# Performance work log

Measured on AMD Instinct MI355X. Metric: run time of the kernel, lower is better.

## Reference

```python
import jax, jax.numpy as jnp
import numpy as np

# Model dims (see init_kwargs)
E = 512        # embedding_dim
H = 1536       # hidden_dim
SIZE = 4       # state_space.size (state types per layer)
S = 32         # choices per state type (uniform state size)
L = 12         # num_layers of child network
T = SIZE * L   # total controller steps = 48
V = SIZE * S   # num_embeddings = 128


def setup_inputs() -> dict:
    key = jax.random.key(0)
    ks = jax.random.split(key, 12)
    sc = 0.05
    f32 = jnp.float32
    return {
        "input_id": 0,
        "emb":   (jax.random.normal(ks[0], (V, E)) * sc).astype(f32),
        "W_ih1": (jax.random.normal(ks[1], (4 * H, E)) * sc).astype(f32),
        "W_hh1": (jax.random.normal(ks[2], (4 * H, H)) * sc).astype(f32),
        "b_ih1": (jax.random.normal(ks[3], (4 * H,)) * sc).astype(f32),
        "b_hh1": (jax.random.normal(ks[4], (4 * H,)) * sc).astype(f32),
        "W_ih2": (jax.random.normal(ks[5], (4 * H, H)) * sc).astype(f32),
        "W_hh2": (jax.random.normal(ks[6], (4 * H, H)) * sc).astype(f32),
        "b_ih2": (jax.random.normal(ks[7], (4 * H,)) * sc).astype(f32),
        "b_hh2": (jax.random.normal(ks[8], (4 * H,)) * sc).astype(f32),
        "W_out": (jax.random.normal(ks[9], (T, S, H)) * sc).astype(f32),
        "b_out": (jax.random.normal(ks[10], (T, S)) * sc).astype(f32),
    }


def _lstm_cell(x, h, c, Wih, Whh, bih, bhh):
    # torch.nn.LSTMCell: gates ordered (i, f, g, o)
    g = x @ Wih.T + bih + h @ Whh.T + bhh
    gi, gf, gg, go = jnp.split(g, 4)
    c_new = jax.nn.sigmoid(gf) * c + jax.nn.sigmoid(gi) * jnp.tanh(gg)
    h_new = jax.nn.sigmoid(go) * jnp.tanh(c_new)
    return h_new, c_new


def reference(input_id, emb, W_ih1, W_hh1, b_ih1, b_hh1,
              W_ih2, W_hh2, b_ih2, b_hh2, W_out, b_out):
    x0 = emb[input_id]                      # [E]
    z = jnp.zeros((H,), emb.dtype)

    def step(carry, inp):
        i, Wo, bo = inp                     # Wo: [S,H], bo: [S]
        x, h1, c1, h2, c2 = carry
        h1, c1 = _lstm_cell(x, h1, c1, W_ih1, W_hh1, b_ih1, b_hh1)
        h2, c2 = _lstm_cell(h1, h2, c2, W_ih2, W_hh2, b_ih2, b_hh2)
        logp = jax.nn.log_softmax(Wo @ h2 + bo)   # [S]
        pred = jnp.argmax(logp)
        emb_id = (i % SIZE) * S + pred            # state-space embedding id
        x_next = emb[emb_id]
        return (x_next, h1, c1, h2, c2), logp

    _, scores = jax.lax.scan(step, (x0, z, z, z, z),
                             (jnp.arange(T), W_out, b_out))
    return scores  # [T, S] log-probabilities
```

## Files before the change

### kernel.cpp

```cpp
#include <hip/hip_runtime.h>
#include <math.h>

#define H 1536
#define E 512
#define T 48
#define S 32
#define V 128
#define NB 256
#define BT 512
#define JPB 6
#define ROWS 24
#define RPW 3
#define CHK 24
#define WHH2_B   (64 * 145 * 16)
#define HBUF_B   (64 * 7 * 16)
#define DYN_LDS  (WHH2_B + HBUF_B)

__device__ __forceinline__ float sigf(float x) { return 1.0f / (1.0f + expf(-x)); }
__device__ __forceinline__ float wred(float acc) {
#pragma unroll
    for (int off = 32; off; off >>= 1) acc += __shfl_down(acc, off);
    return acc;
}

#define GLD(p)    __hip_atomic_load((p), __ATOMIC_RELAXED, __HIP_MEMORY_SCOPE_AGENT)
#define GST(p, v) __hip_atomic_store((p), (v), __ATOMIC_RELAXED, __HIP_MEMORY_SCOPE_AGENT)

__device__ __forceinline__ void gbar(unsigned* flags, unsigned* rel, unsigned& gen) {
    __syncthreads();
    gen++;
    if (blockIdx.x == 0) {
        if (threadIdx.x < 64) {
            const int i0 = threadIdx.x * 4;
            for (;;) {
                unsigned a0 = (i0 == 0) ? gen : GLD(&flags[(i0 + 0) * 16]);
                unsigned a1 = GLD(&flags[(i0 + 1) * 16]);
                unsigned a2 = GLD(&flags[(i0 + 2) * 16]);
                unsigned a3 = GLD(&flags[(i0 + 3) * 16]);
                bool ok = (a0 >= gen) && (a1 >= gen) && (a2 >= gen) && (a3 >= gen);
                if (__all(ok)) break;
                __builtin_amdgcn_s_sleep(1);
            }
#pragma unroll
            for (int k = 0; k < 4; ++k) GST(&rel[(i0 + k) * 16], gen);
        }
    } else {
        if (threadIdx.x == 0) {
            GST(&flags[blockIdx.x * 16], gen);
            while (GLD(&rel[blockIdx.x * 16]) < gen) __builtin_amdgcn_s_sleep(1);
        }
    }
    __syncthreads();
}

__global__ void init_kernel(unsigned* u) {
    for (int i = threadIdx.x; i < 8192; i += 256) u[i] = 0u;
}

__global__ __launch_bounds__(BT, 2) void nas_persist(
    const int* __restrict__ input_id, const float* __restrict__ emb,
    const float* __restrict__ Wih1, const float* __restrict__ Whh1,
    const float* __restrict__ bih1, const float* __restrict__ bhh1,
    const float* __restrict__ Wih2, const float* __restrict__ Whh2,
    const float* __restrict__ bih2, const float* __restrict__ bhh2,
    const float* __restrict__ Wout, const float* __restrict__ bout,
    float* __restrict__ out, float* __restrict__ ws)
{
    const int b = blockIdx.x, tid = threadIdx.x;
    const int wave = tid >> 6, lane = tid & 63;

    unsigned* rel   = (unsigned*)ws;
    unsigned* flags = (unsigned*)ws + 4096;
    float* h2gp[2]  = { ws + 8192, ws + 8192 + H };
    float* candp[2] = { ws + 16384, ws + 16384 + S * H };
    float* xw1g = ws + 114688 + (size_t)b * (V * ROWS);

    extern __shared__ char dyn_lds[];
    float4* whh2s = (float4*)dyn_lds;
    float*  hbuf  = (float*)(dyn_lds + WHH2_B);

    __shared__ float gacc1[ROWS], gaccH[ROWS], g2f[ROWS], bsum2[ROWS], zlog[S];
    __shared__ float c1s[JPB], c2s[JPB], c1cand[S * JPB];
    __shared__ int   xid_s, pred_s;

    unsigned gen = 0;

    if (tid < JPB) { c2s[tid] = 0.f; GST(h2gp[0] + b * JPB + tid, 0.f); }
    if (tid < ROWS) {
        int r = (tid / JPB) * H + b * JPB + (tid % JPB);
        bsum2[tid] = bih2[r] + bhh2[r];
        gaccH[tid] = 0.f;
    }
    if (tid == 0) xid_s = *input_id;

    {
        const int k0 = wave * RPW;
        float4 wiA[RPW], wiB[RPW];
        float  bs[RPW];
#pragma unroll
        for (int i = 0; i < RPW; ++i) {
            int k = k0 + i;
            int r = (k / JPB) * H + b * JPB + (k % JPB);
            const float4* w = (const float4*)(Wih1 + (size_t)r * E);
            wiA[i] = w[lane]; wiB[i] = w[lane + 64];
            bs[i]  = bih1[r] + bhh1[r];
        }
        float4* stage = (float4*)dyn_lds;
        for (int ch = 0; ch < 8; ++ch) {
            const float4* src = (const float4*)(emb + (size_t)ch * 16 * E);
            for (int m = tid; m < 2048; m += BT) stage[m] = src[m];
            __syncthreads();
            for (int vv = 0; vv < 16; ++vv) {
                float4 ea = stage[vv * 128 + lane];
                float4 eb = stage[vv * 128 + 64 + lane];
#pragma unroll
                for (int i = 0; i < RPW; ++i) {
                    float a = wiA[i].x * ea.x + wiA[i].y * ea.y + wiA[i].z * ea.z + wiA[i].w * ea.w
                            + wiB[i].x * eb.x + wiB[i].y * eb.y + wiB[i].z * eb.z + wiB[i].w * eb.w;
                    a = wred(a);
                    if (lane == 0) xw1g[(ch * 16 + vv) * ROWS + (k0 + i)] = a + bs[i];
                }
            }
            __syncthreads();
        }
    }

    for (int k = 0; k < ROWS; ++k) {
        int r = (k / JPB) * H + b * JPB + (k % JPB);
        const float4* src = (const float4*)(Whh2 + (size_t)r * H);
        if (tid < 384) {
            int l = tid / 6, j = tid % 6;
            whh2s[l * 145 + k * 6 + j] = src[tid];
        }
    }
    __syncthreads();

    float w1[RPW][CHK], w2[RPW][CHK];
#pragma unroll
    for (int i = 0; i < RPW; ++i) {
        int k = wave * RPW + i;
        int r = (k / JPB) * H + b * JPB + (k % JPB);
        const float4* p1 = (const float4*)(Whh1 + (size_t)r * H) + lane * 6;
        const float4* p2 = (const float4*)(Wih2 + (size_t)r * H) + lane * 6;
#pragma unroll
        for (int j = 0; j < 6; ++j) {
            float4 v1 = p1[j], v2 = p2[j];
            w1[i][4 * j + 0] = v1.x; w1[i][4 * j + 1] = v1.y;
            w1[i][4 * j + 2] = v1.z; w1[i][4 * j + 3] = v1.w;
            w2[i][4 * j + 0] = v2.x; w2[i][4 * j + 1] = v2.y;
            w2[i][4 * j + 2] = v2.z; w2[i][4 * j + 3] = v2.w;
        }
    }
    __syncthreads();

    if (tid < JPB) {
        const float* xr = xw1g + (size_t)xid_s * ROWS;
        float gi = xr[tid], gg = xr[2 * JPB + tid], go = xr[3 * JPB + tid];
        float cn = sigf(gi) * tanhf(gg);
        c1s[tid] = cn;
        GST(candp[0] + b * JPB + tid, sigf(go) * tanhf(cn));
    }
    gbar(flags, rel, gen);

    for (int k = 0; k <= T; ++k) {
        {
            const float* src = h2gp[k & 1];
            for (int i = tid; i < H; i += BT)
                hbuf[(i / CHK) * 28 + (i % CHK)] = GLD(src + i);
        }
        __syncthreads();
        float h2c[CHK];
        {
            const float4* hp = (const float4*)hbuf + lane * 7;
#pragma unroll
            for (int j = 0; j < 6; ++j) {
                float4 v = hp[j];
                h2c[4 * j + 0] = v.x; h2c[4 * j + 1] = v.y;
                h2c[4 * j + 2] = v.z; h2c[4 * j + 3] = v.w;
            }
        }
        __syncthreads();

        int psel = 0;
        if (k > 0) {
#pragma unroll
            for (int q = 0; q < 4; ++q) {
                int s = wave * 4 + q;
                const float4* wo = (const float4*)(Wout + ((size_t)(k - 1) * S + s) * H) + lane * 6;
                float acc = 0.f;
#pragma unroll
                for (int j = 0; j < 6; ++j) {
                    float4 v = wo[j];
                    acc += v.x * h2c[4 * j + 0] + v.y * h2c[4 * j + 1]
                         + v.z * h2c[4 * j + 2] + v.w * h2c[4 * j + 3];
                }
                acc = wred(acc);
                if (lane == 0) zlog[s] = acc + bout[(k - 1) * S + s];
            }
#pragma unroll
            for (int i = 0; i < RPW; ++i) {
                int kk = wave * RPW + i;
                const float4* wp = whh2s + lane * 145 + kk * 6;
                float ah = 0.f;
#pragma unroll
                for (int j = 0; j < 6; ++j) {
                    float4 v = wp[j];
                    ah += v.x * h2c[4 * j + 0] + v.y * h2c[4 * j + 1]
                        + v.z * h2c[4 * j + 2] + v.w * h2c[4 * j + 3];
                }
                ah = wred(ah);
                if (lane == 0) gaccH[kk] = ah;
            }
            __syncthreads();
            if (wave == 0) {
                float z = (lane < S) ? zlog[lane] : -1e30f;
                float v = z; int idx = (lane < S) ? lane : 9999;
#pragma unroll
                for (int off = 32; off; off >>= 1) {
                    float ov = __shfl_xor(v, off); int oi = __shfl_xor(idx, off);
                    if (ov > v || (ov == v && oi < idx)) { v = ov; idx = oi; }
                }
                float e = (lane < S) ? expf(z - v) : 0.f;
#pragma unroll
                for (int off = 32; off; off >>= 1) e += __shfl_xor(e, off);
                if (lane == 0) pred_s = idx;
                if (b == 0 && lane < S) out[(size_t)(k - 1) * S + lane] = z - v - logf(e);
            }
            __syncthreads();
            if (k == T) return;
            psel = pred_s;
            if (tid < JPB) c1s[tid] = c1cand[psel * JPB + tid];
        }

        {
            const float* src = candp[k & 1] + (size_t)psel * H;
            for (int i = tid; i < H; i += BT)
                hbuf[(i / CHK) * 28 + (i % CHK)] = GLD(src + i);
        }
        __syncthreads();
        float h1c[CHK];
        {
            const float4* hp = (const float4*)hbuf + lane * 7;
#pragma unroll
            for (int j = 0; j < 6; ++j) {
                float4 v = hp[j];
                h1c[4 * j + 0] = v.x; h1c[4 * j + 1] = v.y;
                h1c[4 * j + 2] = v.z; h1c[4 * j + 3] = v.w;
            }
        }
        float a1[RPW], a2[RPW];
#pragma unroll
        for (int i = 0; i < RPW; ++i) { a1[i] = 0.f; a2[i] = 0.f; }
#pragma unroll
        for (int kk = 0; kk < CHK; ++kk) {
            float h = h1c[kk];
#pragma unroll
            for (int i = 0; i < RPW; ++i) {
                a1[i] += w1[i][kk] * h;
                a2[i] += w2[i][kk] * h;
            }
        }
#pragma unroll
        for (int i = 0; i < RPW; ++i) {
            int kk = wave * RPW + i;
            float s1 = wred(a1[i]);
            float s2 = wred(a2[i]);
            if (lane == 0) {
                gacc1[kk] = s1;
                g2f[kk]   = s2 + gaccH[kk] + bsum2[kk];
            }
        }
        __syncthreads();

        if (tid < JPB) {
            float gi = g2f[tid],           gf = g2f[JPB + tid];
            float gg = g2f[2 * JPB + tid], go = g2f[3 * JPB + tid];
            float cn = sigf(gf) * c2s[tid] + sigf(gi) * tanhf(gg);
            c2s[tid] = cn;
            GST(h2gp[(k + 1) & 1] + b * JPB + tid, sigf(go) * tanhf(cn));
        }
        if (tid < S * JPB) {
            int p = tid / JPB, j = tid % JPB;
            const float* xr = xw1g + (size_t)((k & 3) * S + p) * ROWS;
            float gi = gacc1[j]           + xr[j];
            float gf = gacc1[JPB + j]     + xr[JPB + j];
            float gg = gacc1[2 * JPB + j] + xr[2 * JPB + j];
            float go = gacc1[3 * JPB + j] + xr[3 * JPB + j];
            float cn = sigf(gf) * c1s[j] + sigf(gi) * tanhf(gg);
            c1cand[tid] = cn;
            GST(candp[(k + 1) & 1] + (size_t)p * H + b * JPB + j,
                sigf(go) * tanhf(cn));
        }
        gbar(flags, rel, gen);
    }
}

extern "C" void kernel_launch(void* const* d_in, const int* in_sizes, int n_in,
                              void* d_out, int out_size, void* d_ws, size_t ws_size,
                              hipStream_t stream) {
    const int*   input_id = (const int*)d_in[0];
    const float* emb  = (const float*)d_in[1];
    const float* Wih1 = (const float*)d_in[2];
    const float* Whh1 = (const float*)d_in[3];
    const float* bih1 = (const float*)d_in[4];
    const float* bhh1 = (const float*)d_in[5];
    const float* Wih2 = (const float*)d_in[6];
    const float* Whh2 = (const float*)d_in[7];
    const float* bih2 = (const float*)d_in[8];
    const float* bhh2 = (const float*)d_in[9];
    const float* Wout = (const float*)d_in[10];
    const float* bout = (const float*)d_in[11];
    float* out = (float*)d_out;
    float* ws  = (float*)d_ws;

    init_kernel<<<1, 256, 0, stream>>>((unsigned*)ws);

    void* args[] = { (void*)&input_id, (void*)&emb,
                     (void*)&Wih1, (void*)&Whh1, (void*)&bih1, (void*)&bhh1,
                     (void*)&Wih2, (void*)&Whh2, (void*)&bih2, (void*)&bhh2,
                     (void*)&Wout, (void*)&bout, (void*)&out, (void*)&ws };
    hipLaunchCooperativeKernel((void*)nas_persist, dim3(NB), dim3(BT), args,
                               DYN_LDS, stream);
}
```

Baseline: 1.183 ms.

## Use all-to-all flag barrier and distribute output logits as per-block partials

Replaces the master-block gather/release grid barrier with a symmetric barrier in which every block posts its flag and polls all flags directly. This removes one round trip through block 0 per step. The output-logit matvec is split so each block computes partial dot products over its own six h2 elements and publishes them to a double-buffered workspace. After the barrier the partials are summed, so the redundant full Wout·h2 matvec in every block goes away. Global loads of h2 and the h1 candidate are issued early and held in registers to overlap latency, and Whh2·h2 now stays in registers instead of shared memory. The costs are 256 blocks polling 256 flags each, which adds memory traffic, plus an extra workspace region and one more syncthreads.

```diff
diff --git a/kernel.cpp b/kernel.cpp
--- a/kernel.cpp
+++ b/kernel.cpp
@@ -26,28 +26,20 @@
 #define GLD(p)    __hip_atomic_load((p), __ATOMIC_RELAXED, __HIP_MEMORY_SCOPE_AGENT)
 #define GST(p, v) __hip_atomic_store((p), (v), __ATOMIC_RELAXED, __HIP_MEMORY_SCOPE_AGENT)
 
-__device__ __forceinline__ void gbar(unsigned* flags, unsigned* rel, unsigned& gen) {
+__device__ __forceinline__ void gbar(unsigned* flags, unsigned& gen) {
     __syncthreads();
     gen++;
-    if (blockIdx.x == 0) {
-        if (threadIdx.x < 64) {
-            const int i0 = threadIdx.x * 4;
-            for (;;) {
-                unsigned a0 = (i0 == 0) ? gen : GLD(&flags[(i0 + 0) * 16]);
-                unsigned a1 = GLD(&flags[(i0 + 1) * 16]);
-                unsigned a2 = GLD(&flags[(i0 + 2) * 16]);
-                unsigned a3 = GLD(&flags[(i0 + 3) * 16]);
-                bool ok = (a0 >= gen) && (a1 >= gen) && (a2 >= gen) && (a3 >= gen);
-                if (__all(ok)) break;
-                __builtin_amdgcn_s_sleep(1);
-            }
-#pragma unroll
-            for (int k = 0; k < 4; ++k) GST(&rel[(i0 + k) * 16], gen);
-        }
-    } else {
-        if (threadIdx.x == 0) {
-            GST(&flags[blockIdx.x * 16], gen);
-            while (GLD(&rel[blockIdx.x * 16]) < gen) __builtin_amdgcn_s_sleep(1);
+    if (threadIdx.x == 0) GST(&flags[blockIdx.x * 16], gen);
+    if (threadIdx.x < 64) {
+        const int i0 = threadIdx.x * 4;
+        for (;;) {
+            unsigned a0 = GLD(&flags[(i0 + 0) * 16]);
+            unsigned a1 = GLD(&flags[(i0 + 1) * 16]);
+            unsigned a2 = GLD(&flags[(i0 + 2) * 16]);
+            unsigned a3 = GLD(&flags[(i0 + 3) * 16]);
+            bool ok = (a0 >= gen) && (a1 >= gen) && (a2 >= gen) && (a3 >= gen);
+            if (__all(ok)) break;
+            __builtin_amdgcn_s_sleep(1);
         }
     }
     __syncthreads();
@@ -69,17 +61,17 @@
     const int b = blockIdx.x, tid = threadIdx.x;
     const int wave = tid >> 6, lane = tid & 63;
 
-    unsigned* rel   = (unsigned*)ws;
     unsigned* flags = (unsigned*)ws + 4096;
     float* h2gp[2]  = { ws + 8192, ws + 8192 + H };
     float* candp[2] = { ws + 16384, ws + 16384 + S * H };
     float* xw1g = ws + 114688 + (size_t)b * (V * ROWS);
+    float* logitp = ws + 901120;
 
     extern __shared__ char dyn_lds[];
     float4* whh2s = (float4*)dyn_lds;
     float*  hbuf  = (float*)(dyn_lds + WHH2_B);
 
-    __shared__ float gacc1[ROWS], gaccH[ROWS], g2f[ROWS], bsum2[ROWS], zlog[S];
+    __shared__ float gacc1[ROWS], g2f[ROWS], bsum2[ROWS], zlog[S], h2f[JPB];
     __shared__ float c1s[JPB], c2s[JPB], c1cand[S * JPB];
     __shared__ int   xid_s, pred_s;
 
@@ -89,7 +81,6 @@
     if (tid < ROWS) {
         int r = (tid / JPB) * H + b * JPB + (tid % JPB);
         bsum2[tid] = bih2[r] + bhh2[r];
-        gaccH[tid] = 0.f;
     }
     if (tid == 0) xid_s = *input_id;
 
@@ -160,58 +151,37 @@
         c1s[tid] = cn;
         GST(candp[0] + b * JPB + tid, sigf(go) * tanhf(cn));
     }
-    gbar(flags, rel, gen);
+    gbar(flags, gen);
+
+    const int m0 = (tid / CHK) * 28 + (tid % CHK);
+    const int m1 = ((tid + 512) / CHK) * 28 + ((tid + 512) % CHK);
+    const int m2 = ((tid + 1024) / CHK) * 28 + ((tid + 1024) % CHK);
 
     for (int k = 0; k <= T; ++k) {
-        {
-            const float* src = h2gp[k & 1];
-            for (int i = tid; i < H; i += BT)
-                hbuf[(i / CHK) * 28 + (i % CHK)] = GLD(src + i);
-        }
-        __syncthreads();
-        float h2c[CHK];
-        {
-            const float4* hp = (const float4*)hbuf + lane * 7;
-#pragma unroll
-            for (int j = 0; j < 6; ++j) {
-                float4 v = hp[j];
-                h2c[4 * j + 0] = v.x; h2c[4 * j + 1] = v.y;
-                h2c[4 * j + 2] = v.z; h2c[4 * j + 3] = v.w;
-            }
-        }
-        __syncthreads();
-
-        int psel = 0;
+        float wcol[JPB];
+        if (k < T && wave == 0 && lane < S) {
+            const float* wp = Wout + ((size_t)k * S + lane) * H + b * JPB;
+#pragma unroll
+            for (int j = 0; j < JPB; ++j) wcol[j] = wp[j];
+        }
+        const float* h2src = h2gp[k & 1];
+        float u0 = GLD(h2src + tid);
+        float u1 = GLD(h2src + tid + 512);
+        float u2 = GLD(h2src + tid + 1024);
+
         if (k > 0) {
-#pragma unroll
-            for (int q = 0; q < 4; ++q) {
-                int s = wave * 4 + q;
-                const float4* wo = (const float4*)(Wout + ((size_t)(k - 1) * S + s) * H) + lane * 6;
-                float acc = 0.f;
-#pragma unroll
-                for (int j = 0; j < 6; ++j) {
-                    float4 v = wo[j];
-                    acc += v.x * h2c[4 * j + 0] + v.y * h2c[4 * j + 1]
-                         + v.z * h2c[4 * j + 2] + v.w * h2c[4 * j + 3];
-                }
-                acc = wred(acc);
-                if (lane == 0) zlog[s] = acc + bout[(k - 1) * S + s];
-            }
-#pragma unroll
-            for (int i = 0; i < RPW; ++i) {
-                int kk = wave * RPW + i;
-                const float4* wp = whh2s + lane * 145 + kk * 6;
-                float ah = 0.f;
-#pragma unroll
-                for (int j = 0; j < 6; ++j) {
-                    float4 v = wp[j];
-                    ah += v.x * h2c[4 * j + 0] + v.y * h2c[4 * j + 1]
-                        + v.z * h2c[4 * j + 2] + v.w * h2c[4 * j + 3];
-                }
-                ah = wred(ah);
-                if (lane == 0) gaccH[kk] = ah;
-            }
-            __syncthreads();
+            const float* lp = logitp + (size_t)(k & 1) * (S * NB)
+                              + (tid >> 4) * NB + (tid & 15) * 16;
+            float acc = 0.f;
+#pragma unroll
+            for (int i = 0; i < 16; ++i) acc += GLD(lp + i);
+#pragma unroll
+            for (int off = 8; off; off >>= 1) acc += __shfl_down(acc, off, 16);
+            if ((tid & 15) == 0)
+                zlog[tid >> 4] = acc + bout[(size_t)(k - 1) * S + (tid >> 4)];
+        }
+        __syncthreads();
+        if (k > 0) {
             if (wave == 0) {
                 float z = (lane < S) ? zlog[lane] : -1e30f;
                 float v = z; int idx = (lane < S) ? lane : 9999;
@@ -227,16 +197,44 @@
                 if (b == 0 && lane < S) out[(size_t)(k - 1) * S + lane] = z - v - logf(e);
             }
             __syncthreads();
-            if (k == T) return;
-            psel = pred_s;
-            if (tid < JPB) c1s[tid] = c1cand[psel * JPB + tid];
-        }
-
+        }
+        if (k == T) return;
+        const int psel = (k > 0) ? pred_s : 0;
+        if (k > 0 && tid < JPB) c1s[tid] = c1cand[psel * JPB + tid];
+
+        const float* h1src = candp[k & 1] + (size_t)psel * H;
+        float t0 = GLD(h1src + tid);
+        float t1 = GLD(h1src + tid + 512);
+        float t2 = GLD(h1src + tid + 1024);
+
+        hbuf[m0] = u0; hbuf[m1] = u1; hbuf[m2] = u2;
+        __syncthreads();
+        float h2c[CHK];
         {
-            const float* src = candp[k & 1] + (size_t)psel * H;
-            for (int i = tid; i < H; i += BT)
-                hbuf[(i / CHK) * 28 + (i % CHK)] = GLD(src + i);
-        }
+            const float4* hp = (const float4*)hbuf + lane * 7;
+#pragma unroll
+            for (int j = 0; j < 6; ++j) {
+                float4 v = hp[j];
+                h2c[4 * j + 0] = v.x; h2c[4 * j + 1] = v.y;
+                h2c[4 * j + 2] = v.z; h2c[4 * j + 3] = v.w;
+            }
+        }
+        float ahv[RPW];
+#pragma unroll
+        for (int i = 0; i < RPW; ++i) {
+            int kk = wave * RPW + i;
+            const float4* wp = whh2s + lane * 145 + kk * 6;
+            float ah = 0.f;
+#pragma unroll
+            for (int j = 0; j < 6; ++j) {
+                float4 v = wp[j];
+                ah += v.x * h2c[4 * j + 0] + v.y * h2c[4 * j + 1]
+                    + v.z * h2c[4 * j + 2] + v.w * h2c[4 * j + 3];
+            }
+            ahv[i] = wred(ah);
+        }
+        __syncthreads();
+        hbuf[m0] = t0; hbuf[m1] = t1; hbuf[m2] = t2;
         __syncthreads();
         float h1c[CHK];
         {
@@ -267,7 +265,7 @@
             float s2 = wred(a2[i]);
             if (lane == 0) {
                 gacc1[kk] = s1;
-                g2f[kk]   = s2 + gaccH[kk] + bsum2[kk];
+                g2f[kk]   = s2 + ahv[i] + bsum2[kk];
             }
         }
         __syncthreads();
@@ -277,7 +275,9 @@
             float gg = g2f[2 * JPB + tid], go = g2f[3 * JPB + tid];
             float cn = sigf(gf) * c2s[tid] + sigf(gi) * tanhf(gg);
             c2s[tid] = cn;
-            GST(h2gp[(k + 1) & 1] + b * JPB + tid, sigf(go) * tanhf(cn));
+            float hn = sigf(go) * tanhf(cn);
+            h2f[tid] = hn;
+            GST(h2gp[(k + 1) & 1] + b * JPB + tid, hn);
         }
         if (tid < S * JPB) {
             int p = tid / JPB, j = tid % JPB;
@@ -291,7 +291,14 @@
             GST(candp[(k + 1) & 1] + (size_t)p * H + b * JPB + j,
                 sigf(go) * tanhf(cn));
         }
-        gbar(flags, rel, gen);
+        __syncthreads();
+        if (wave == 0 && lane < S) {
+            float p = 0.f;
+#pragma unroll
+            for (int j = 0; j < JPB; ++j) p += wcol[j] * h2f[j];
+            GST(logitp + (size_t)((k + 1) & 1) * (S * NB) + lane * NB + b, p);
+        }
+        gbar(flags, gen);
     }
 }
 
```

After: 1.147 ms, median of 2. 1.03x faster.
